# Kernel tuning notes

Hardware: AMD Instinct MI355X
Metric: run time of the kernel (lower is better)

The kernel has to match this reference:

```python
import jax, jax.numpy as jnp
import numpy as np

D_MODEL = 2048
NUM_HEADS = 32
HEAD_DIM = D_MODEL // NUM_HEADS  # 64
ROPE_BASE = 10000.0


def _rope_cos_sin(seq_len, head_dim, dtype):
    inv_freq = 1.0 / (ROPE_BASE ** (jnp.arange(0, head_dim, 2, dtype=jnp.float32) / head_dim))
    freqs = jnp.arange(seq_len, dtype=jnp.float32)[:, None] * inv_freq[None, :]  # (S, Dh/2)
    emb = jnp.concatenate([freqs, freqs], axis=-1)  # (S, Dh)
    return emb.astype(dtype), jnp.cos(emb).astype(dtype), jnp.sin(emb).astype(dtype)


def _rotate_half(x):
    x1, x2 = jnp.split(x, 2, axis=-1)
    return jnp.concatenate([-x2, x1], axis=-1)


def setup_inputs() -> dict:
    key = jax.random.key(0)
    k1, k2, k3, k4 = jax.random.split(key, 4)
    B, S, D = 1, 2048, D_MODEL
    x = jax.random.normal(k1, (B, S, D), dtype=jnp.float32)
    Wqkv = jax.random.normal(k2, (3 * D, D), dtype=jnp.float32) * 0.02
    Wo = jax.random.normal(k3, (D, D), dtype=jnp.float32) * 0.02
    gate = jax.random.normal(k4, (D,), dtype=jnp.float32) * 0.1
    return {"x": x, "Wqkv": Wqkv, "Wo": Wo, "gate": gate}


def reference(x, Wqkv, Wo, gate):
    B, S, D = x.shape
    H, Dh = NUM_HEADS, HEAD_DIM
    residual = x

    # fused QKV projection (torch Linear: y = x @ W.T)
    qkv = jnp.einsum('bsd,ed->bse', x, Wqkv).reshape(B, S, 3, H, Dh)
    q, k, v = qkv[:, :, 0], qkv[:, :, 1], qkv[:, :, 2]  # each (B, S, H, Dh)

    # RoPE
    _, cos, sin = _rope_cos_sin(S, Dh, x.dtype)
    cos = cos[None, :, None, :]  # (1, S, 1, Dh)
    sin = sin[None, :, None, :]
    q = q * cos + _rotate_half(q) * sin
    k = k * cos + _rotate_half(k) * sin

    # causal SDPA
    scale = 1.0 / np.sqrt(Dh)
    scores = jnp.einsum('bqhd,bkhd->bhqk', q, k) * scale  # (B, H, S, S)
    causal = jnp.tril(jnp.ones((S, S), dtype=bool))
    scores = jnp.where(causal[None, None], scores, jnp.finfo(scores.dtype).min)
    probs = jax.nn.softmax(scores, axis=-1)
    attn = jnp.einsum('bhqk,bkhd->bqhd', probs, v).reshape(B, S, D)

    out = jnp.einsum('bsd,ed->bse', attn, Wo)
    # HeoGate: learned per-channel gated residual (assumption; see notes)
    return residual + gate * out
```

## Files before the change

### kernel.cpp

```cpp
#include <hip/hip_runtime.h>
#include <hip/hip_bf16.h>
#include <cstdint>
#include <cstddef>

typedef __hip_bfloat16 bf16;
typedef short short8 __attribute__((ext_vector_type(8)));
typedef float f32x4 __attribute__((ext_vector_type(4)));

#define S_LEN 2048
#define DMODEL 2048
#define NQKV 6144
#define NHEADS 32
#define HDIM 64
#define ROPE_L2 0.4152410118609203f
#define Q_PRESCALE 0.18033688011112042f

__device__ __forceinline__ void async_copy16(const bf16* g, bf16* l) {
  __builtin_amdgcn_global_load_lds(
      (const __attribute__((address_space(1))) void*)g,
      (__attribute__((address_space(3))) void*)l, 16, 0, 0);
}

__device__ __forceinline__ f32x4 mfma_bf16(short8 a, short8 b, f32x4 c) {
  return __builtin_amdgcn_mfma_f32_16x16x32_bf16(a, b, c, 0, 0, 0);
}

__global__ __launch_bounds__(256) void cvt3_kernel(const float* __restrict__ sx,
                                                   bf16* __restrict__ dx,
                                                   const float* __restrict__ sw,
                                                   bf16* __restrict__ dw,
                                                   const float* __restrict__ so,
                                                   bf16* __restrict__ dov) {
  int i = blockIdx.x * 256 + threadIdx.x;
  const float* s;
  bf16* d;
  if (i < 1048576) {
    s = sx; d = dx;
  } else if (i < 4194304) {
    s = sw; d = dw; i -= 1048576;
  } else {
    s = so; d = dov; i -= 4194304;
  }
  const float4 v = ((const float4*)s)[i];
  union { bf16 h[4]; ushort4 u; } tmp;
  tmp.h[0] = __float2bfloat16(v.x);
  tmp.h[1] = __float2bfloat16(v.y);
  tmp.h[2] = __float2bfloat16(v.z);
  tmp.h[3] = __float2bfloat16(v.w);
  ((ushort4*)d)[i] = tmp.u;
}

#define QKV_NT 32
#define QBAR() do { __builtin_amdgcn_s_barrier(); __builtin_amdgcn_sched_barrier(0); } while (0)
#define WAITV(n) asm volatile("s_waitcnt vmcnt(" #n ")" ::: "memory")
#define LGKM0() do { asm volatile("s_waitcnt lgkmcnt(0)" ::: "memory"); \
                     __builtin_amdgcn_sched_barrier(0); } while (0)

__global__ __launch_bounds__(256, 2) void gemm_qkv(const bf16* __restrict__ A,
                                                   const bf16* __restrict__ W,
                                                   bf16* __restrict__ q_ws,
                                                   bf16* __restrict__ k_ws,
                                                   bf16* __restrict__ v_ws) {
  __shared__ bf16 smem[32768];
  const int tid = threadIdx.x;
  const int wave = tid >> 6, lane = tid & 63;
  const int wm = wave >> 1, wn = wave & 1;
  const int srow = tid >> 2;
  const int swc = (((tid & 3) ^ ((tid >> 3) & 3)) * 8);
  const int fr = lane & 15, fq = lane >> 4;
  const int rdc = ((fq ^ ((fr >> 1) & 3)) * 8);

  const int b = blockIdx.x;
  const int nrep = (b < 256) ? 2 : 1;

  const bf16 *Asrc, *Bsrc;
  auto stage = [&](int t_, int bufe_) {
#pragma unroll
    for (int kk = 0; kk < 2; ++kk) {
      const int ko = t_ * 64 + kk * 32;
      async_copy16(Asrc + ko, &smem[bufe_ + kk * 4096 + wave * 512]);
      async_copy16(Asrc + (size_t)64 * DMODEL + ko,
                   &smem[bufe_ + kk * 4096 + 2048 + wave * 512]);
      async_copy16(Bsrc + ko, &smem[bufe_ + 8192 + kk * 4096 + wave * 512]);
      async_copy16(Bsrc + (size_t)64 * DMODEL + ko,
                   &smem[bufe_ + 8192 + kk * 4096 + 2048 + wave * 512]);
    }
  };

  const f32x4 zero = {0.f, 0.f, 0.f, 0.f};
  f32x4 acc[4][4];
  short8 a0[4], a1[4], b0[4], b1[4];

  for (int rep = 0; rep < nrep; ++rep) {
    const int tile = (rep == 0) ? b : (512 + b);
    const int m0 = (tile / 48) * 128, n0 = (tile % 48) * 128;
    Asrc = A + (size_t)(m0 + srow) * DMODEL + swc;
    Bsrc = W + (size_t)(n0 + srow) * DMODEL + swc;

#pragma unroll
    for (int i = 0; i < 4; ++i)
#pragma unroll
      for (int j = 0; j < 4; ++j) acc[i][j] = zero;

    if (rep) __syncthreads();

    stage(0, 0);
    stage(1, 16384);
    WAITV(8);
    QBAR();

#pragma unroll 2
    for (int t = 0; t < QKV_NT; ++t) {
      const int bc = (t & 1) * 16384;
#pragma unroll
      for (int mi = 0; mi < 4; ++mi) {
        const int ro = (wm * 64 + mi * 16 + fr) * 32 + rdc;
        a0[mi] = *(const short8*)&smem[bc + ro];
        a1[mi] = *(const short8*)&smem[bc + 4096 + ro];
      }
#pragma unroll
      for (int n = 0; n < 4; ++n) {
        const int ro = (wn * 64 + n * 16 + fr) * 32 + rdc;
        b0[n] = *(const short8*)&smem[bc + 8192 + ro];
        b1[n] = *(const short8*)&smem[bc + 12288 + ro];
      }
      LGKM0();
      QBAR();
      if (t + 2 < QKV_NT) stage(t + 2, bc);
      __builtin_amdgcn_s_setprio(1);
#pragma unroll
      for (int mi = 0; mi < 4; ++mi)
#pragma unroll
        for (int n = 0; n < 4; ++n)
          acc[mi][n] = mfma_bf16(a0[mi], b0[n], acc[mi][n]);
#pragma unroll
      for (int mi = 0; mi < 4; ++mi)
#pragma unroll
        for (int n = 0; n < 4; ++n)
          acc[mi][n] = mfma_bf16(a1[mi], b1[n], acc[mi][n]);
      __builtin_amdgcn_s_setprio(0);
      if (t + 2 < QKV_NT)      { WAITV(8); }
      else if (t + 1 < QKV_NT) { WAITV(0); }
      QBAR();
    }

    const int colb = n0 + wn * 64;
    const int sect = colb >> 11;
    const int h = (colb & 2047) >> 6;
    const int col = fr, rq = fq * 4;

    if (sect < 2) {
      bf16* dst = ((sect == 0) ? q_ws : k_ws) + (size_t)h * S_LEN * HDIM;
      bf16* rep_b = smem + wave * 1152;
      const float qs = (sect == 0) ? Q_PRESCALE : 1.0f;
      const float f0 = exp2f(-(float)col * ROPE_L2);
      const float f1 = exp2f(-(float)(16 + col) * ROPE_L2);
      __syncthreads();
      for (int m = 0; m < 4; ++m) {
        const int base_s = m0 + wm * 64 + m * 16;
#pragma unroll
        for (int jl = 0; jl < 2; ++jl) {
          const int dh = jl * 16 + col;
          const float fr_ = (jl == 0) ? f0 : f1;
#pragma unroll
          for (int r = 0; r < 4; ++r) {
            const int srw = base_s + rq + r;
            float sn, cs;
            __sincosf((float)srw * fr_, &sn, &cs);
            const float xl = acc[m][jl][r], xh = acc[m][jl + 2][r];
            rep_b[(rq + r) * 72 + dh]      = __float2bfloat16((xl * cs - xh * sn) * qs);
            rep_b[(rq + r) * 72 + dh + 32] = __float2bfloat16((xh * cs + xl * sn) * qs);
          }
        }
#pragma unroll
        for (int p = 0; p < 2; ++p) {
          const int rr = p * 8 + (lane >> 3), ch = lane & 7;
          const uint4 vv = *(const uint4*)&rep_b[rr * 72 + ch * 8];
          *(uint4*)&dst[(size_t)(base_s + rr) * HDIM + ch * 8] = vv;
        }
      }
    } else {
      bf16* dst = v_ws + (size_t)h * HDIM * S_LEN;
      for (int j = 0; j < 4; ++j) {
        const int dh = j * 16 + col;
        for (int m = 0; m < 4; ++m) {
          const int s0 = m0 + wm * 64 + m * 16 + rq;
          union { bf16 hx[4]; uint2 u; } vk;
#pragma unroll
          for (int r = 0; r < 4; ++r) vk.hx[r] = __float2bfloat16(acc[m][j][r]);
          *(uint2*)&dst[(size_t)dh * S_LEN + s0] = vk.u;
        }
      }
    }
  }
}

__global__ __launch_bounds__(512) void attn_kernel(const bf16* __restrict__ q_ws,
                                                   const bf16* __restrict__ k_ws,
                                                   const bf16* __restrict__ vt_ws,
                                                   bf16* __restrict__ attn_out) {
  const int bid = blockIdx.x;
  const int qt = 15 - (bid >> 5);
  const int h = bid & 31;

  const int tid = threadIdx.x, wave = tid >> 6, lane = tid & 63;
  const int col = lane & 15, fq = lane >> 4;
  const int q_glob = qt * 128 + wave * 16 + col;

  __shared__ bf16 Ks[2][64 * 64];
  __shared__ bf16 Vs[2][64 * 64];
  __shared__ bf16 Pl[8][16 * 72];
  bf16* pl = Pl[wave];

  const bf16* qh = q_ws + (size_t)h * S_LEN * HDIM;
  const bf16* kh = k_ws + (size_t)h * S_LEN * HDIM;
  const bf16* vh = vt_ws + (size_t)h * HDIM * S_LEN;

  const int srow = lane >> 3;
  const int slot = lane & 7;
  const int schunk = slot ^ srow;

  auto stage = [&](int kt, int buf) {
    const int k0 = kt * 64;
    const int r8 = wave * 8;
    async_copy16(kh + (size_t)(k0 + r8 + srow) * HDIM + schunk * 8,
                 &Ks[buf][r8 * 64]);
    async_copy16(vh + (size_t)(r8 + srow) * S_LEN + k0 + schunk * 8,
                 &Vs[buf][r8 * 64]);
  };

  short8 qf[2];
#pragma unroll
  for (int ks = 0; ks < 2; ++ks)
    qf[ks] = *(const short8*)&qh[(size_t)q_glob * HDIM + ks * 32 + fq * 8];

  const f32x4 zero = {0.f, 0.f, 0.f, 0.f};
  f32x4 o_acc[4] = {zero, zero, zero, zero};
  float m_i = -1e30f, l_i = 0.f;

  stage(0, 0);

  const int lastk = 2 * qt + 1;
  for (int kt = 0; kt <= lastk; ++kt) {
    const int buf = kt & 1;
    const int k0 = kt * 64;
    __syncthreads();
    if (kt < lastk) stage(kt + 1, buf ^ 1);

    short8 kf[8];
#pragma unroll
    for (int n = 0; n < 4; ++n) {
      const int row = n * 16 + col;
#pragma unroll
      for (int ks = 0; ks < 2; ++ks)
        kf[n * 2 + ks] =
            *(const short8*)&Ks[buf][row * 64 + (((ks * 4 + fq) ^ (row & 7)) * 8)];
    }
    f32x4 s_acc[4] = {zero, zero, zero, zero};
#pragma unroll
    for (int n = 0; n < 4; ++n)
#pragma unroll
      for (int ks = 0; ks < 2; ++ks)
        s_acc[n] = mfma_bf16(kf[n * 2 + ks], qf[ks], s_acc[n]);

    short8 vf[8];
#pragma unroll
    for (int n = 0; n < 4; ++n) {
      const int row = n * 16 + col;
#pragma unroll
      for (int ks = 0; ks < 2; ++ks)
        vf[n * 2 + ks] =
            *(const short8*)&Vs[buf][row * 64 + (((ks * 4 + fq) ^ (row & 7)) * 8)];
    }

    if (k0 + 63 > qt * 128 + wave * 16) {
#pragma unroll
      for (int n = 0; n < 4; ++n)
#pragma unroll
        for (int r = 0; r < 4; ++r)
          if (k0 + n * 16 + fq * 4 + r > q_glob) s_acc[n][r] = -1e30f;
    }

    float vmax = -1e30f;
#pragma unroll
    for (int n = 0; n < 4; ++n)
#pragma unroll
      for (int r = 0; r < 4; ++r) vmax = fmaxf(vmax, s_acc[n][r]);
    vmax = fmaxf(vmax, __shfl_xor(vmax, 16, 64));
    vmax = fmaxf(vmax, __shfl_xor(vmax, 32, 64));

    if (!__all(vmax - m_i <= 8.0f)) {
      const float mnew = fmaxf(m_i, vmax);
      const float alpha = exp2f(m_i - mnew);
      l_i *= alpha;
#pragma unroll
      for (int n = 0; n < 4; ++n)
#pragma unroll
        for (int r = 0; r < 4; ++r) o_acc[n][r] *= alpha;
      m_i = mnew;
    }

    float rs = 0.f;
#pragma unroll
    for (int n = 0; n < 4; ++n)
#pragma unroll
      for (int r = 0; r < 4; ++r) {
        const float p = exp2f(s_acc[n][r] - m_i);
        s_acc[n][r] = p;
        rs += p;
      }
    rs += __shfl_xor(rs, 16, 64);
    rs += __shfl_xor(rs, 32, 64);
    l_i += rs;

#pragma unroll
    for (int n = 0; n < 4; ++n) {
      union { bf16 hx[4]; uint2 u; } pk;
#pragma unroll
      for (int r = 0; r < 4; ++r) pk.hx[r] = __float2bfloat16(s_acc[n][r]);
      *(uint2*)&pl[col * 72 + n * 16 + fq * 4] = pk.u;
    }
    short8 pa[2];
#pragma unroll
    for (int ks = 0; ks < 2; ++ks)
      pa[ks] = *(const short8*)&pl[col * 72 + ks * 32 + fq * 8];

#pragma unroll
    for (int n = 0; n < 4; ++n)
#pragma unroll
      for (int ks = 0; ks < 2; ++ks)
        o_acc[n] = mfma_bf16(vf[n * 2 + ks], pa[ks], o_acc[n]);
  }

  const float inv = 1.0f / l_i;
#pragma unroll
  for (int n = 0; n < 4; ++n) {
#pragma unroll
    for (int r = 0; r < 4; ++r) o_acc[n][r] *= inv;
    union { bf16 hx[4]; uint2 u; } ok;
#pragma unroll
    for (int r = 0; r < 4; ++r) ok.hx[r] = __float2bfloat16(o_acc[n][r]);
    *(uint2*)&attn_out[(size_t)q_glob * DMODEL + h * HDIM + n * 16 + fq * 4] = ok.u;
  }
}

__global__ __launch_bounds__(512, 2) void gemm_out(const bf16* __restrict__ A,
                                                   const bf16* __restrict__ W,
                                                   const float* __restrict__ xres,
                                                   const float* __restrict__ gate,
                                                   float* __restrict__ out) {
  constexpr int K = DMODEL;
  constexpr int NT = K / 64;
  __shared__ bf16 smem[32768];
  const int tid = threadIdx.x;
  const int wave = tid >> 6, lane = tid & 63;
  const int wm = wave >> 2, wn = wave & 3;
  const int m0 = blockIdx.y * 128, n0 = blockIdx.x * 128;
  const int srow = tid >> 2;
  const int swc = (((tid & 3) ^ ((tid >> 3) & 3)) * 8);
  const int fr = lane & 15, fq = lane >> 4;
  const int rdc = ((fq ^ ((fr >> 1) & 3)) * 8);

  const bf16* Asrc = A + (size_t)(m0 + srow) * K + swc;
  const bf16* Bsrc = W + (size_t)(n0 + srow) * K + swc;

  auto stage = [&](int t_, int bufe_) {
#pragma unroll
    for (int kk = 0; kk < 2; ++kk) {
      const int ko = t_ * 64 + kk * 32;
      async_copy16(Asrc + ko, &smem[bufe_ + kk * 4096 + wave * 512]);
      async_copy16(Bsrc + ko, &smem[bufe_ + 8192 + kk * 4096 + wave * 512]);
    }
  };

  const f32x4 zero = {0.f, 0.f, 0.f, 0.f};
  f32x4 acc[4][2];
#pragma unroll
  for (int i = 0; i < 4; ++i)
#pragma unroll
    for (int j = 0; j < 2; ++j) acc[i][j] = zero;
  short8 a0[4], a1[4], b0[2], b1[2];

  stage(0, 0);
  stage(1, 16384);
  WAITV(4);
  QBAR();

  for (int t = 0; t < NT; ++t) {
    const int bc = (t & 1) * 16384;
#pragma unroll
    for (int i = 0; i < 4; ++i) {
      const int ro = (wm * 64 + i * 16 + fr) * 32 + rdc;
      a0[i] = *(const short8*)&smem[bc + ro];
      a1[i] = *(const short8*)&smem[bc + 4096 + ro];
    }
#pragma unroll
    for (int j = 0; j < 2; ++j) {
      const int ro = (wn * 32 + j * 16 + fr) * 32 + rdc;
      b0[j] = *(const short8*)&smem[bc + 8192 + ro];
      b1[j] = *(const short8*)&smem[bc + 12288 + ro];
    }
    LGKM0();
    QBAR();
    if (t + 2 < NT) stage(t + 2, bc);
    __builtin_amdgcn_s_setprio(1);
#pragma unroll
    for (int i = 0; i < 4; ++i)
#pragma unroll
      for (int j = 0; j < 2; ++j)
        acc[i][j] = mfma_bf16(a0[i], b0[j], acc[i][j]);
#pragma unroll
    for (int i = 0; i < 4; ++i)
#pragma unroll
      for (int j = 0; j < 2; ++j)
        acc[i][j] = mfma_bf16(a1[i], b1[j], acc[i][j]);
    __builtin_amdgcn_s_setprio(0);
    if (t + 2 < NT)      { WAITV(4); }
    else if (t + 1 < NT) { WAITV(0); }
    QBAR();
  }

  const int col = fr, rq = fq * 4;
  for (int j = 0; j < 2; ++j) {
    const int cc = n0 + wn * 32 + j * 16 + col;
    const float g = gate[cc];
    for (int i = 0; i < 4; ++i) {
      const int base_row = m0 + wm * 64 + i * 16 + rq;
      for (int r = 0; r < 4; ++r) {
        const size_t idx = (size_t)(base_row + r) * DMODEL + cc;
        out[idx] = xres[idx] + g * acc[i][j][r];
      }
    }
  }
}

extern "C" void kernel_launch(void* const* d_in, const int* in_sizes, int n_in,
                              void* d_out, int out_size, void* d_ws, size_t ws_size,
                              hipStream_t stream) {
  const float* x    = (const float*)d_in[0];
  const float* Wqkv = (const float*)d_in[1];
  const float* Wo   = (const float*)d_in[2];
  const float* gate = (const float*)d_in[3];
  float* out = (float*)d_out;

  char* ws = (char*)d_ws;
  const size_t MB = 1024 * 1024;
  bf16* xb      = (bf16*)(ws);
  bf16* wqkvb   = (bf16*)(ws + 8 * MB);
  bf16* wob     = (bf16*)(ws + 32 * MB);
  bf16* q_ws    = (bf16*)(ws + 40 * MB);
  bf16* k_ws    = (bf16*)(ws + 48 * MB);
  bf16* v_ws    = (bf16*)(ws + 56 * MB);
  bf16* attn_ws = (bf16*)(ws);

  cvt3_kernel<<<dim3(20480), 256, 0, stream>>>(x, xb, Wqkv, wqkvb, Wo, wob);

  gemm_qkv<<<dim3(512), 256, 0, stream>>>(xb, wqkvb, q_ws, k_ws, v_ws);
  attn_kernel<<<dim3(512), 512, 0, stream>>>(q_ws, k_ws, v_ws, attn_ws);
  gemm_out<<<dim3(DMODEL / 128, DMODEL / 128), 512, 0, stream>>>(attn_ws, wob, x, gate, out);
}
```

Measured before the change: 247.4 us.

## Split attention KV tiles across wave pairs with 32-query waves and merge partials

The attention kernel now processes 128-key stages. Waves are split into two groups, each handling half of the keys (a split-K) for 32 queries per wave, which reuses each K/V fragment load across two query groups. At the end the partial softmax states (m, l, O) of the two groups are merged through shared memory. This aims to cut LDS traffic per MFMA and the number of barriers per key, in exchange for more registers, a larger shared footprint, and a final reduction step. Initial m is changed to -1e9 so fully masked partials merge safely.

```diff
diff --git a/kernel.cpp b/kernel.cpp
--- a/kernel.cpp
+++ b/kernel.cpp
@@ -195,152 +195,215 @@
   }
 }
 
-__global__ __launch_bounds__(512) void attn_kernel(const bf16* __restrict__ q_ws,
-                                                   const bf16* __restrict__ k_ws,
-                                                   const bf16* __restrict__ vt_ws,
-                                                   bf16* __restrict__ attn_out) {
+__global__ __launch_bounds__(512, 2) void attn_kernel(const bf16* __restrict__ q_ws,
+                                                      const bf16* __restrict__ k_ws,
+                                                      const bf16* __restrict__ vt_ws,
+                                                      bf16* __restrict__ attn_out) {
   const int bid = blockIdx.x;
   const int qt = 15 - (bid >> 5);
   const int h = bid & 31;
 
   const int tid = threadIdx.x, wave = tid >> 6, lane = tid & 63;
+  const int wq = wave & 3, wk = wave >> 2;
   const int col = lane & 15, fq = lane >> 4;
-  const int q_glob = qt * 128 + wave * 16 + col;
-
-  __shared__ bf16 Ks[2][64 * 64];
-  __shared__ bf16 Vs[2][64 * 64];
-  __shared__ bf16 Pl[8][16 * 72];
-  bf16* pl = Pl[wave];
+  const int qbase = qt * 128 + wq * 32;
+
+  __shared__ __align__(16) bf16 smem[51200];
+  bf16* KS = smem;
+  bf16* VS = smem + 16384;
+  bf16* pl = smem + 32768 + wave * 2304;
 
   const bf16* qh = q_ws + (size_t)h * S_LEN * HDIM;
   const bf16* kh = k_ws + (size_t)h * S_LEN * HDIM;
   const bf16* vh = vt_ws + (size_t)h * HDIM * S_LEN;
 
   const int srow = lane >> 3;
-  const int slot = lane & 7;
-  const int schunk = slot ^ srow;
-
-  auto stage = [&](int kt, int buf) {
-    const int k0 = kt * 64;
-    const int r8 = wave * 8;
-    async_copy16(kh + (size_t)(k0 + r8 + srow) * HDIM + schunk * 8,
-                 &Ks[buf][r8 * 64]);
-    async_copy16(vh + (size_t)(r8 + srow) * S_LEN + k0 + schunk * 8,
-                 &Vs[buf][r8 * 64]);
+  const int schunk = (lane & 7) ^ srow;
+
+  auto stage = [&](int ss, int buf) {
+    const int k0 = ss * 128;
+#pragma unroll
+    for (int j = 0; j < 2; ++j) {
+      const int kr = j * 64 + wave * 8 + srow;
+      async_copy16(kh + (size_t)(k0 + kr) * HDIM + schunk * 8,
+                   &KS[buf * 8192 + (j * 64 + wave * 8) * 64]);
+    }
+#pragma unroll
+    for (int j = 0; j < 2; ++j) {
+      const int dh = j * 32 + wave * 4 + (lane >> 4);
+      const int cg = (lane & 15) ^ (dh & 7);
+      async_copy16(vh + (size_t)dh * S_LEN + k0 + cg * 8,
+                   &VS[buf * 8192 + (j * 32 + wave * 4) * 128]);
+    }
   };
 
-  short8 qf[2];
-#pragma unroll
-  for (int ks = 0; ks < 2; ++ks)
-    qf[ks] = *(const short8*)&qh[(size_t)q_glob * HDIM + ks * 32 + fq * 8];
+  short8 qf[2][2];
+#pragma unroll
+  for (int g = 0; g < 2; ++g)
+#pragma unroll
+    for (int ks = 0; ks < 2; ++ks)
+      qf[g][ks] = *(const short8*)&qh[(size_t)(qbase + g * 16 + col) * HDIM +
+                                      ks * 32 + fq * 8];
 
   const f32x4 zero = {0.f, 0.f, 0.f, 0.f};
-  f32x4 o_acc[4] = {zero, zero, zero, zero};
-  float m_i = -1e30f, l_i = 0.f;
+  f32x4 o_acc[2][4];
+#pragma unroll
+  for (int g = 0; g < 2; ++g)
+#pragma unroll
+    for (int n = 0; n < 4; ++n) o_acc[g][n] = zero;
+  float m_i[2] = {-1e9f, -1e9f}, l_i[2] = {0.f, 0.f};
 
   stage(0, 0);
 
-  const int lastk = 2 * qt + 1;
-  for (int kt = 0; kt <= lastk; ++kt) {
-    const int buf = kt & 1;
-    const int k0 = kt * 64;
+  for (int ss = 0; ss <= qt; ++ss) {
+    const int buf = ss & 1;
     __syncthreads();
-    if (kt < lastk) stage(kt + 1, buf ^ 1);
+    if (ss < qt) stage(ss + 1, buf ^ 1);
+
+    const int k0 = ss * 128 + wk * 64;
 
     short8 kf[8];
 #pragma unroll
     for (int n = 0; n < 4; ++n) {
-      const int row = n * 16 + col;
+      const int r = wk * 64 + n * 16 + col;
 #pragma unroll
       for (int ks = 0; ks < 2; ++ks)
         kf[n * 2 + ks] =
-            *(const short8*)&Ks[buf][row * 64 + (((ks * 4 + fq) ^ (row & 7)) * 8)];
-    }
-    f32x4 s_acc[4] = {zero, zero, zero, zero};
-#pragma unroll
-    for (int n = 0; n < 4; ++n)
-#pragma unroll
-      for (int ks = 0; ks < 2; ++ks)
-        s_acc[n] = mfma_bf16(kf[n * 2 + ks], qf[ks], s_acc[n]);
+            *(const short8*)&KS[buf * 8192 + r * 64 + (((ks * 4 + fq) ^ (r & 7)) * 8)];
+    }
+    f32x4 s_acc[2][4];
+#pragma unroll
+    for (int g = 0; g < 2; ++g)
+#pragma unroll
+      for (int n = 0; n < 4; ++n) s_acc[g][n] = zero;
+#pragma unroll
+    for (int g = 0; g < 2; ++g)
+#pragma unroll
+      for (int n = 0; n < 4; ++n)
+#pragma unroll
+        for (int ks = 0; ks < 2; ++ks)
+          s_acc[g][n] = mfma_bf16(kf[n * 2 + ks], qf[g][ks], s_acc[g][n]);
 
     short8 vf[8];
 #pragma unroll
     for (int n = 0; n < 4; ++n) {
-      const int row = n * 16 + col;
+      const int dh = n * 16 + col;
 #pragma unroll
       for (int ks = 0; ks < 2; ++ks)
         vf[n * 2 + ks] =
-            *(const short8*)&Vs[buf][row * 64 + (((ks * 4 + fq) ^ (row & 7)) * 8)];
-    }
-
-    if (k0 + 63 > qt * 128 + wave * 16) {
+            *(const short8*)&VS[buf * 8192 + dh * 128 +
+                                (((wk * 8 + ks * 4 + fq) ^ (dh & 7)) * 8)];
+    }
+
+    if (k0 + 63 > qbase) {
+#pragma unroll
+      for (int g = 0; g < 2; ++g) {
+        const int qg = qbase + g * 16 + col;
+#pragma unroll
+        for (int n = 0; n < 4; ++n)
+#pragma unroll
+          for (int r = 0; r < 4; ++r)
+            if (k0 + n * 16 + fq * 4 + r > qg) s_acc[g][n][r] = -1e30f;
+      }
+    }
+
+#pragma unroll
+    for (int g = 0; g < 2; ++g) {
+      float vmax = -1e30f;
 #pragma unroll
       for (int n = 0; n < 4; ++n)
 #pragma unroll
+        for (int r = 0; r < 4; ++r) vmax = fmaxf(vmax, s_acc[g][n][r]);
+      vmax = fmaxf(vmax, __shfl_xor(vmax, 16, 64));
+      vmax = fmaxf(vmax, __shfl_xor(vmax, 32, 64));
+
+      if (!__all(vmax - m_i[g] <= 8.0f)) {
+        const float mnew = fmaxf(m_i[g], vmax);
+        const float alpha = exp2f(m_i[g] - mnew);
+        l_i[g] *= alpha;
+#pragma unroll
+        for (int n = 0; n < 4; ++n)
+#pragma unroll
+          for (int r = 0; r < 4; ++r) o_acc[g][n][r] *= alpha;
+        m_i[g] = mnew;
+      }
+
+      float rs = 0.f;
+#pragma unroll
+      for (int n = 0; n < 4; ++n)
+#pragma unroll
+        for (int r = 0; r < 4; ++r) {
+          const float p = exp2f(s_acc[g][n][r] - m_i[g]);
+          s_acc[g][n][r] = p;
+          rs += p;
+        }
+      rs += __shfl_xor(rs, 16, 64);
+      rs += __shfl_xor(rs, 32, 64);
+      l_i[g] += rs;
+
+#pragma unroll
+      for (int n = 0; n < 4; ++n) {
+        union { bf16 hx[4]; uint2 u; } pk;
+#pragma unroll
+        for (int r = 0; r < 4; ++r) pk.hx[r] = __float2bfloat16(s_acc[g][n][r]);
+        *(uint2*)&pl[(g * 16 + col) * 72 + n * 16 + fq * 4] = pk.u;
+      }
+    }
+
+    short8 pa[2][2];
+#pragma unroll
+    for (int g = 0; g < 2; ++g)
+#pragma unroll
+      for (int ks = 0; ks < 2; ++ks)
+        pa[g][ks] = *(const short8*)&pl[(g * 16 + col) * 72 + ks * 32 + fq * 8];
+
+#pragma unroll
+    for (int g = 0; g < 2; ++g)
+#pragma unroll
+      for (int n = 0; n < 4; ++n)
+#pragma unroll
+        for (int ks = 0; ks < 2; ++ks)
+          o_acc[g][n] = mfma_bf16(vf[n * 2 + ks], pa[g][ks], o_acc[g][n]);
+  }
+
+  __syncthreads();
+  float* fo = (float*)smem;
+  float* fm = (float*)(smem + 16384);
+  if (wave >= 4) {
+    const int off = ((wave - 4) * 64 + lane) * 32;
+#pragma unroll
+    for (int g = 0; g < 2; ++g)
+#pragma unroll
+      for (int n = 0; n < 4; ++n)
+        *(f32x4*)&fo[off + (g * 4 + n) * 4] = o_acc[g][n];
+    const int moff = ((wave - 4) * 64 + lane) * 4;
+    fm[moff + 0] = m_i[0];
+    fm[moff + 1] = l_i[0];
+    fm[moff + 2] = m_i[1];
+    fm[moff + 3] = l_i[1];
+  }
+  __syncthreads();
+  if (wave < 4) {
+    const int off = (wave * 64 + lane) * 32;
+    const int moff = (wave * 64 + lane) * 4;
+#pragma unroll
+    for (int g = 0; g < 2; ++g) {
+      const float mB = fm[moff + g * 2], lB = fm[moff + g * 2 + 1];
+      const float m = fmaxf(m_i[g], mB);
+      const float a = exp2f(m_i[g] - m), bsc = exp2f(mB - m);
+      const float l = l_i[g] * a + lB * bsc;
+      const float inv = 1.0f / l;
+      const int qg = qbase + g * 16 + col;
+#pragma unroll
+      for (int n = 0; n < 4; ++n) {
+        const f32x4 oB = *(const f32x4*)&fo[off + (g * 4 + n) * 4];
+        union { bf16 hx[4]; uint2 u; } ok;
+#pragma unroll
         for (int r = 0; r < 4; ++r)
-          if (k0 + n * 16 + fq * 4 + r > q_glob) s_acc[n][r] = -1e30f;
-    }
-
-    float vmax = -1e30f;
-#pragma unroll
-    for (int n = 0; n < 4; ++n)
-#pragma unroll
-      for (int r = 0; r < 4; ++r) vmax = fmaxf(vmax, s_acc[n][r]);
-    vmax = fmaxf(vmax, __shfl_xor(vmax, 16, 64));
-    vmax = fmaxf(vmax, __shfl_xor(vmax, 32, 64));
-
-    if (!__all(vmax - m_i <= 8.0f)) {
-      const float mnew = fmaxf(m_i, vmax);
-      const float alpha = exp2f(m_i - mnew);
-      l_i *= alpha;
-#pragma unroll
-      for (int n = 0; n < 4; ++n)
-#pragma unroll
-        for (int r = 0; r < 4; ++r) o_acc[n][r] *= alpha;
-      m_i = mnew;
-    }
-
-    float rs = 0.f;
-#pragma unroll
-    for (int n = 0; n < 4; ++n)
-#pragma unroll
-      for (int r = 0; r < 4; ++r) {
-        const float p = exp2f(s_acc[n][r] - m_i);
-        s_acc[n][r] = p;
-        rs += p;
-      }
-    rs += __shfl_xor(rs, 16, 64);
-    rs += __shfl_xor(rs, 32, 64);
-    l_i += rs;
-
-#pragma unroll
-    for (int n = 0; n < 4; ++n) {
-      union { bf16 hx[4]; uint2 u; } pk;
-#pragma unroll
-      for (int r = 0; r < 4; ++r) pk.hx[r] = __float2bfloat16(s_acc[n][r]);
-      *(uint2*)&pl[col * 72 + n * 16 + fq * 4] = pk.u;
-    }
-    short8 pa[2];
-#pragma unroll
-    for (int ks = 0; ks < 2; ++ks)
-      pa[ks] = *(const short8*)&pl[col * 72 + ks * 32 + fq * 8];
-
-#pragma unroll
-    for (int n = 0; n < 4; ++n)
-#pragma unroll
-      for (int ks = 0; ks < 2; ++ks)
-        o_acc[n] = mfma_bf16(vf[n * 2 + ks], pa[ks], o_acc[n]);
-  }
-
-  const float inv = 1.0f / l_i;
-#pragma unroll
-  for (int n = 0; n < 4; ++n) {
-#pragma unroll
-    for (int r = 0; r < 4; ++r) o_acc[n][r] *= inv;
-    union { bf16 hx[4]; uint2 u; } ok;
-#pragma unroll
-    for (int r = 0; r < 4; ++r) ok.hx[r] = __float2bfloat16(o_acc[n][r]);
-    *(uint2*)&attn_out[(size_t)q_glob * DMODEL + h * HDIM + n * 16 + fq * 4] = ok.u;
+          ok.hx[r] = __float2bfloat16((o_acc[g][n][r] * a + oB[r] * bsc) * inv);
+        *(uint2*)&attn_out[(size_t)qg * DMODEL + h * HDIM + n * 16 + fq * 4] = ok.u;
+      }
+    }
   }
 }
 
```

Result: faster. 242.0 us (median of 3 runs) (-2.2%).
